# Kernel optimization log

Hardware: AMD Instinct MI355X
Metric: run time of the kernel (lower is better)

Reference implementation:

```python
import jax, jax.numpy as jnp
import numpy as np
from jax import lax

B, N_PER = 8, 4096          # clouds, points per cloud (batch vector is uniform)
RATIO, RADIUS, K = 0.25, 0.2, 64
N_SAMPLE = int(N_PER * RATIO)
C_IN, H = 64, 128               # input feature dim, MLP hidden/out dim


def setup_inputs() -> dict:
    key = jax.random.key(0)
    k = jax.random.split(key, 6)
    N = B * N_PER
    x = jax.random.normal(k[0], (N, C_IN), jnp.float32)
    pos = jax.random.uniform(k[1], (N, 3), jnp.float32)
    batch = jnp.repeat(jnp.arange(B, dtype=jnp.int32), N_PER)
    s1 = 1.0 / np.sqrt(C_IN + 3)
    s2 = 1.0 / np.sqrt(H)
    W1 = jax.random.uniform(k[2], (C_IN + 3, H), jnp.float32, -s1, s1)
    b1 = jax.random.uniform(k[3], (H,), jnp.float32, -s1, s1)
    W2 = jax.random.uniform(k[4], (H, H), jnp.float32, -s2, s2)
    b2 = jax.random.uniform(k[5], (H,), jnp.float32, -s2, s2)
    return {"x": x, "pos": pos, "W1": W1, "b1": b1, "W2": W2, "b2": b2, "batch": batch}


def _fps(pos_c):
    # Farthest point sampling on one cloud [n,3] -> [N_SAMPLE] int32 indices.
    # Sequential by nature: scan over sample steps, vectorized over all points.
    def step(carry, _):
        mind, last = carry
        d = jnp.sum((pos_c - pos_c[last]) ** 2, axis=-1)
        mind = jnp.minimum(mind, d)
        nxt = jnp.argmax(mind).astype(jnp.int32)
        return (mind, nxt), nxt

    init = (jnp.full((pos_c.shape[0],), 1e10, jnp.float32), jnp.int32(0))
    _, idxs = lax.scan(step, init, None, length=N_SAMPLE - 1)
    return jnp.concatenate([jnp.zeros((1,), jnp.int32), idxs])


def reference(x, pos, W1, b1, W2, b2, batch):
    # batch is uniform (N_PER points per cloud) so the flat [N,*] tensors
    # reshape to [B, N_PER, *]; this honors the per-batch fps/radius semantics.
    pos_b = pos.reshape(B, N_PER, 3)
    x_b = x.reshape(B, N_PER, C_IN)

    idx = jax.vmap(_fps)(pos_b)                                    # [B,S]
    pos_c = jnp.take_along_axis(pos_b, idx[..., None], axis=1)     # [B,S,3]

    # radius ball query: K nearest within RADIUS (cap max_num_neighbors=64)
    d2 = jnp.sum((pos_c[:, :, None, :] - pos_b[:, None, :, :]) ** 2, axis=-1)  # [B,S,n]
    neg_d, nbr = lax.top_k(-d2, K)                                 # [B,S,K]
    valid = (-neg_d) <= RADIUS ** 2                                # center itself always valid

    # gather neighbor features/positions via flat global indices
    gidx = (nbr + (jnp.arange(B, dtype=nbr.dtype) * N_PER)[:, None, None]).reshape(-1)
    x_j = x.reshape(B * N_PER, C_IN)[gidx].reshape(B, N_SAMPLE, K, C_IN)
    pos_j = pos.reshape(B * N_PER, 3)[gidx].reshape(B, N_SAMPLE, K, 3)

    # PointNetConv message: local_nn(concat(x_j, pos_j - pos_i)), max aggregation
    feat = jnp.concatenate([x_j, pos_j - pos_c[:, :, None, :]], axis=-1)  # [B,S,K,C_IN+3]
    h = jax.nn.relu(feat @ W1 + b1)
    h = jax.nn.relu(h @ W2 + b2)                                   # [B,S,K,H]
    h = jnp.where(valid[..., None], h, -1e9)
    x_out = jnp.max(h, axis=2).reshape(B * N_SAMPLE, H)

    pos_out = pos_c.reshape(B * N_SAMPLE, 3)
    batch_out = jnp.repeat(jnp.arange(B, dtype=jnp.int32), N_SAMPLE)
    return x_out, pos_out, batch_out
```

## Files before the change

kernel.cpp:

```cpp
#include <hip/hip_runtime.h>

#define NB 8
#define N_PER 4096
#define N_SAMPLE 1024
#define KNN 64
#define CIN 64
#define HD 128
#define R2F 0.04f
#define LIST_CAP 384
#define STR 136

typedef __attribute__((ext_vector_type(8))) short bf16x8;
typedef __attribute__((ext_vector_type(4))) float f32x4;

__device__ __forceinline__ unsigned short f2bf(float f) {
    const unsigned u = __float_as_uint(f);
    return (unsigned short)((u + 0x7fff + ((u >> 16) & 1)) >> 16);
}

template <int CTRL>
__device__ __forceinline__ unsigned long long dpp_shift_u64(unsigned long long k) {
    const unsigned lo = (unsigned)k;
    const unsigned hi = (unsigned)(k >> 32);
    const unsigned olo =
        (unsigned)__builtin_amdgcn_update_dpp(0, (int)lo, CTRL, 0xf, 0xf, false);
    const unsigned ohi =
        (unsigned)__builtin_amdgcn_update_dpp(0, (int)hi, CTRL, 0xf, 0xf, false);
    return ((unsigned long long)ohi << 32) | olo;
}
__device__ __forceinline__ unsigned long long wave_max_u64(unsigned long long k) {
    unsigned long long o;
    o = dpp_shift_u64<0x111>(k); k = o > k ? o : k;
    o = dpp_shift_u64<0x112>(k); k = o > k ? o : k;
    o = dpp_shift_u64<0x114>(k); k = o > k ? o : k;
    o = dpp_shift_u64<0x118>(k); k = o > k ? o : k;
    o = dpp_shift_u64<0x142>(k); k = o > k ? o : k;
    o = dpp_shift_u64<0x143>(k); k = o > k ? o : k;
    return k;
}

template <int CTRL, int RMASK>
__device__ __forceinline__ int dpp_add_step(int v) {
    const int o = __builtin_amdgcn_update_dpp(0, v, CTRL, RMASK, 0xf, false);
    return v + o;
}
__device__ __forceinline__ int wave_incl_scan(int v) {
    v = dpp_add_step<0x111, 0xf>(v);
    v = dpp_add_step<0x112, 0xf>(v);
    v = dpp_add_step<0x114, 0xf>(v);
    v = dpp_add_step<0x118, 0xf>(v);
    v = dpp_add_step<0x142, 0xa>(v);
    v = dpp_add_step<0x143, 0xc>(v);
    return v;
}

#define GBLOCKS ((NB * N_PER) / 2)
__global__ __launch_bounds__(256) void fps_g_kernel(const float* __restrict__ pos,
                                                    const float* __restrict__ x,
                                                    const float* __restrict__ W1,
                                                    const float* __restrict__ b1,
                                                    const float* __restrict__ W2,
                                                    float* __restrict__ g,
                                                    short* __restrict__ w2t,
                                                    int* __restrict__ idx_out,
                                                    float* __restrict__ pos_out,
                                                    float* __restrict__ batch_out) {
    __shared__ float pxyz[N_PER * 3];
    __shared__ __align__(16) unsigned long long pkey[2][4];
    __shared__ int lhist[N_SAMPLE];
    const int t = threadIdx.x;

    if (blockIdx.x >= NB + GBLOCKS) {
        const int base = (int)(blockIdx.x - (NB + GBLOCKS)) * 2048 + t * 8;
#pragma unroll
        for (int i = 0; i < 8; ++i) {
            const int idx = base + i;
            const int n = idx >> 7, k = idx & 127;
            w2t[idx] = (short)f2bf(W2[k * HD + n]);
        }
        return;
    }

    if (blockIdx.x >= NB) {
        const int n0 = (int)(blockIdx.x - NB) * 2;
        if (t < 2 * CIN) pxyz[t] = x[(size_t)n0 * CIN + t];
        if (t < 6) pxyz[512 + t] = pos[(size_t)n0 * 3 + t];
        __syncthreads();
        const int lp = t >> 7;
        const int h = t & 127;
        float acc = b1[h];
        const float* xv = pxyz + lp * CIN;
#pragma unroll 8
        for (int c = 0; c < CIN; ++c) acc += xv[c] * W1[c * HD + h];
        const float* pv = pxyz + 512 + lp * 3;
#pragma unroll
        for (int d = 0; d < 3; ++d) acc += pv[d] * W1[(CIN + d) * HD + h];
        g[(size_t)(n0 + lp) * HD + h] = acc;
        return;
    }

    const int b = blockIdx.x;
    const float* posb = pos + (size_t)b * N_PER * 3;
    for (int i = t; i < N_PER * 3; i += 256) pxyz[i] = posb[i];
    if (t == 0) lhist[0] = 0;
    __syncthreads();

    float rx[16], ry[16], rz[16], mind[16];
#pragma unroll
    for (int k = 0; k < 16; ++k) {
        const int p = t + (k << 8);
        rx[k] = pxyz[p * 3 + 0];
        ry[k] = pxyz[p * 3 + 1];
        rz[k] = pxyz[p * 3 + 2];
        mind[k] = 1e10f;
    }
    int last = 0;

    for (int s = 1; s < N_SAMPLE; ++s) {
        const float* lp3 = pxyz + last * 3;
        const float lx = lp3[0], ly = lp3[1], lz = lp3[2];
        float bv = -1.0f;
        int bi = 0x7fffffff;
#pragma unroll
        for (int k = 0; k < 16; ++k) {
            const float dx = rx[k] - lx;
            const float dy = ry[k] - ly;
            const float dz = rz[k] - lz;
            const float d = __fadd_rn(__fadd_rn(__fmul_rn(dx, dx), __fmul_rn(dy, dy)),
                                      __fmul_rn(dz, dz));
            const float m = fminf(mind[k], d);
            mind[k] = m;
            if (m > bv) { bv = m; bi = t + (k << 8); }
        }
        unsigned long long key =
            ((unsigned long long)__float_as_uint(bv) << 32) | (unsigned)(~bi);
        key = wave_max_u64(key);

        const int par = s & 1;
        if ((t & 63) == 63) pkey[par][t >> 6] = key;
        __syncthreads();
        const ulonglong2* pk2 = (const ulonglong2*)(&pkey[par][0]);
        const ulonglong2 A = pk2[0], Bq = pk2[1];
        unsigned long long f0 = A.x > A.y ? A.x : A.y;
        const unsigned long long f1 = Bq.x > Bq.y ? Bq.x : Bq.y;
        f0 = f0 > f1 ? f0 : f1;
        last = (int)(~(unsigned)f0);
        if (t == (s & 255)) lhist[s] = last;
    }
    __syncthreads();

    for (int i = t; i < N_SAMPLE; i += 256) {
        const int li = lhist[i];
        idx_out[b * N_SAMPLE + i] = b * N_PER + li;
        pos_out[(size_t)(b * N_SAMPLE + i) * 3 + 0] = pxyz[li * 3 + 0];
        pos_out[(size_t)(b * N_SAMPLE + i) * 3 + 1] = pxyz[li * 3 + 1];
        pos_out[(size_t)(b * N_SAMPLE + i) * 3 + 2] = pxyz[li * 3 + 2];
        batch_out[b * N_SAMPLE + i] = (float)b;
    }
}

__global__ __launch_bounds__(256) void main_kernel(const float* __restrict__ pos,
                                                   const float* __restrict__ W1,
                                                   const short* __restrict__ W2T,
                                                   const float* __restrict__ b2,
                                                   const float* __restrict__ g,
                                                   const int* __restrict__ idx_in,
                                                   float* __restrict__ x_out) {
    __shared__ short h1b[KNN * STR];
    __shared__ unsigned long long keys[LIST_CAP + 8];
    __shared__ int sel[KNN];
    __shared__ float pcW[HD];
    __shared__ float cp[3];
    __shared__ __align__(16) int wtot[4];
    __shared__ float stripmax[4][HD];

    const int t = threadIdx.x;
    const int s = blockIdx.x;
    const int b = s >> 10;
    const int gci = idx_in[s];
    if (t < 3) cp[t] = pos[(size_t)gci * 3 + t];
    if (t < KNN) sel[t] = 0;
    __syncthreads();

    if (t < HD) {
        pcW[t] = cp[0] * W1[CIN * HD + t] + cp[1] * W1[(CIN + 1) * HD + t] +
                 cp[2] * W1[(CIN + 2) * HD + t];
    }

    const float cx = cp[0], cy = cp[1], cz = cp[2];
    const size_t base = (size_t)b * N_PER;
    const int lane = t & 63;
    const int w = t >> 6;

    float d2r[16];
    int nh = 0;
#pragma unroll
    for (int k = 0; k < 16; ++k) {
        const int p = t + (k << 8);
        const float* pp = pos + (base + p) * 3;
        const float dx = pp[0] - cx;
        const float dy = pp[1] - cy;
        const float dz = pp[2] - cz;
        const float d2 = __fadd_rn(__fadd_rn(__fmul_rn(dx, dx), __fmul_rn(dy, dy)),
                                   __fmul_rn(dz, dz));
        d2r[k] = d2;
        nh += (d2 <= R2F) ? 1 : 0;
    }
    const int incl = wave_incl_scan(nh);
    if (lane == 63) wtot[w] = incl;
    __syncthreads();
    const int4 wt = *(const int4*)(&wtot[0]);
    const int tot = wt.x + wt.y + wt.z + wt.w;
    int slot = incl - nh;
    if (w > 0) slot += wt.x;
    if (w > 1) slot += wt.y;
    if (w > 2) slot += wt.z;
#pragma unroll
    for (int k = 0; k < 16; ++k) {
        if (d2r[k] <= R2F) {
            if (slot < LIST_CAP)
                keys[slot] = ((unsigned long long)__float_as_uint(d2r[k]) << 32) |
                             (unsigned)(t + (k << 8));
            ++slot;
        }
    }
    const int C = min(tot, LIST_CAP);
    const int Cp = (C + 7) & ~7;
    if (t < Cp - C) keys[C + t] = ~0ull;
    __syncthreads();
    const int M = min(C, KNN);

    for (int e = t; e < C; e += 256) {
        const unsigned long long ke = keys[e];
        int rank = 0;
        for (int q = 0; q < Cp; q += 8) {
#pragma unroll
            for (int j = 0; j < 8; ++j) rank += (keys[q + j] < ke) ? 1 : 0;
        }
        if (rank < KNN) sel[rank] = (int)(ke & 0xFFFFFFFFull);
    }
    __syncthreads();

    for (int lin = t; lin < KNN * (HD / 2); lin += 256) {
        const int m = lin >> 6;
        const int hp = lin & 63;
        float v0 = 0.0f, v1 = 0.0f;
        if (m < M) {
            const float2 gv = *(const float2*)(g + (base + sel[m]) * HD + 2 * hp);
            v0 = fmaxf(gv.x - pcW[2 * hp], 0.0f);
            v1 = fmaxf(gv.y - pcW[2 * hp + 1], 0.0f);
        }
        const unsigned pk = (unsigned)f2bf(v0) | ((unsigned)f2bf(v1) << 16);
        *(unsigned*)(&h1b[m * STR + 2 * hp]) = pk;
    }
    __syncthreads();

    const int row = lane & 15;
    const int kg = lane >> 4;

    bf16x8 afr[4];
#pragma unroll
    for (int kc = 0; kc < 4; ++kc)
        afr[kc] = *(const bf16x8*)(&h1b[(w * 16 + row) * STR + kc * 32 + kg * 8]);

#pragma unroll
    for (int nt = 0; nt < 8; ++nt) {
        f32x4 acc = {0.0f, 0.0f, 0.0f, 0.0f};
#pragma unroll
        for (int kc = 0; kc < 4; ++kc) {
            const bf16x8 bfr =
                *(const bf16x8*)(W2T + (nt * 16 + row) * HD + kc * 32 + kg * 8);
            acc = __builtin_amdgcn_mfma_f32_16x16x32_bf16(afr[kc], bfr, acc, 0, 0, 0);
        }
        const float bb = b2[nt * 16 + row];
        float mxv = -1e9f;
#pragma unroll
        for (int r = 0; r < 4; ++r) {
            const int m = w * 16 + kg * 4 + r;
            const float v = fmaxf(acc[r] + bb, 0.0f);
            if (m < M) mxv = fmaxf(mxv, v);
        }
        mxv = fmaxf(mxv, __shfl_xor(mxv, 16));
        mxv = fmaxf(mxv, __shfl_xor(mxv, 32));
        if (lane < 16) stripmax[w][nt * 16 + lane] = mxv;
    }
    __syncthreads();
    if (t < HD) {
        const float v = fmaxf(fmaxf(stripmax[0][t], stripmax[1][t]),
                              fmaxf(stripmax[2][t], stripmax[3][t]));
        x_out[(size_t)s * HD + t] = v;
    }
}

extern "C" void kernel_launch(void* const* d_in, const int* in_sizes, int n_in,
                              void* d_out, int out_size, void* d_ws, size_t ws_size,
                              hipStream_t stream) {
    const float* x   = (const float*)d_in[0];
    const float* pos = (const float*)d_in[1];
    const float* W1  = (const float*)d_in[2];
    const float* b1  = (const float*)d_in[3];
    const float* W2  = (const float*)d_in[4];
    const float* b2  = (const float*)d_in[5];

    float* out = (float*)d_out;
    float* x_out     = out;
    float* pos_out   = out + (size_t)NB * N_SAMPLE * HD;
    float* batch_out = pos_out + (size_t)NB * N_SAMPLE * 3;

    int*   idx_ws = (int*)d_ws;
    short* w2t    = (short*)((char*)d_ws + 32768);
    float* g      = (float*)((char*)d_ws + 65536);

    fps_g_kernel<<<NB + GBLOCKS + 8, 256, 0, stream>>>(pos, x, W1, b1, W2, g, w2t,
                                                       idx_ws, pos_out, batch_out);
    main_kernel<<<NB * N_SAMPLE, 256, 0, stream>>>(pos, W1, w2t, b2, g, idx_ws, x_out);
}
```

Measured before the change: 844.5 us.

## Fuse FPS and ball-query MLP into one persistent kernel with flag streaming

Merges the two kernels into one persistent launch. Eight blocks run farthest point sampling and publish each sampled center through per-sample global flags, while 500 worker blocks first compute the layer-1 projection g. They then meet at a global counter barrier and consume centers as they appear, interleaved across clouds. Downstream radius/MLP work can therefore overlap the sequential FPS instead of waiting for it to finish. In exchange it adds spin-wait polling, a memset, and a reliance on all blocks being co-resident for the grid barrier to avoid deadlock.

```diff
diff --git a/kernel.cpp b/kernel.cpp
--- a/kernel.cpp
+++ b/kernel.cpp
@@ -9,6 +9,12 @@
 #define R2F 0.04f
 #define LIST_CAP 384
 #define STR 136
+#define NFPS 8
+#define NWK 500
+#define GRID (NFPS + NWK)
+#define GCHUNK 66
+#define NPTS (NB * N_PER)
+#define NTASK (NB * N_SAMPLE)
 
 typedef __attribute__((ext_vector_type(8))) short bf16x8;
 typedef __attribute__((ext_vector_type(4))) float f32x4;
@@ -54,241 +60,268 @@
     return v;
 }
 
-#define GBLOCKS ((NB * N_PER) / 2)
-__global__ __launch_bounds__(256) void fps_g_kernel(const float* __restrict__ pos,
-                                                    const float* __restrict__ x,
-                                                    const float* __restrict__ W1,
-                                                    const float* __restrict__ b1,
-                                                    const float* __restrict__ W2,
-                                                    float* __restrict__ g,
-                                                    short* __restrict__ w2t,
-                                                    int* __restrict__ idx_out,
-                                                    float* __restrict__ pos_out,
-                                                    float* __restrict__ batch_out) {
-    __shared__ float pxyz[N_PER * 3];
-    __shared__ __align__(16) unsigned long long pkey[2][4];
-    __shared__ int lhist[N_SAMPLE];
+union SMem {
+    struct {
+        float pxyz[N_PER * 3];
+        unsigned long long pkey[2][4];
+    } f;
+    struct {
+        unsigned long long keys[LIST_CAP + 8];
+        short h1b[KNN * STR];
+        int sel[KNN];
+        float pcW[HD];
+        float stripmax[4][HD];
+        float gx[2 * CIN];
+        float gp[8];
+        int wtot[4];
+        int bcast;
+    } m;
+};
+
+__global__ __launch_bounds__(256, 2) void fused_kernel(
+    const float* __restrict__ pos, const float* __restrict__ x,
+    const float* __restrict__ W1, const float* __restrict__ b1,
+    const float* __restrict__ W2, const float* __restrict__ b2,
+    float* __restrict__ g, short* __restrict__ w2t, int* __restrict__ flags,
+    unsigned* __restrict__ gdone, float* __restrict__ x_out,
+    float* __restrict__ pos_out, float* __restrict__ batch_out) {
+    __shared__ SMem sm;
     const int t = threadIdx.x;
 
-    if (blockIdx.x >= NB + GBLOCKS) {
-        const int base = (int)(blockIdx.x - (NB + GBLOCKS)) * 2048 + t * 8;
-#pragma unroll
-        for (int i = 0; i < 8; ++i) {
-            const int idx = base + i;
-            const int n = idx >> 7, k = idx & 127;
-            w2t[idx] = (short)f2bf(W2[k * HD + n]);
+    if (blockIdx.x < NFPS) {
+        const int b = blockIdx.x;
+        const float* posb = pos + (size_t)b * N_PER * 3;
+        float* pxyz = sm.f.pxyz;
+        for (int i = t; i < N_PER * 3; i += 256) pxyz[i] = posb[i];
+        __syncthreads();
+
+        float rx[16], ry[16], rz[16], mind[16];
+#pragma unroll
+        for (int k = 0; k < 16; ++k) {
+            const int p = t + (k << 8);
+            rx[k] = pxyz[p * 3 + 0];
+            ry[k] = pxyz[p * 3 + 1];
+            rz[k] = pxyz[p * 3 + 2];
+            mind[k] = 1e10f;
+        }
+        int last = 0;
+        if (t == 0) {
+            __hip_atomic_store(&flags[b * N_SAMPLE], b * N_PER + 1, __ATOMIC_RELAXED,
+                               __HIP_MEMORY_SCOPE_AGENT);
+            pos_out[(size_t)(b * N_SAMPLE) * 3 + 0] = pxyz[0];
+            pos_out[(size_t)(b * N_SAMPLE) * 3 + 1] = pxyz[1];
+            pos_out[(size_t)(b * N_SAMPLE) * 3 + 2] = pxyz[2];
+            batch_out[b * N_SAMPLE] = (float)b;
+        }
+
+        for (int s = 1; s < N_SAMPLE; ++s) {
+            const float* lp3 = pxyz + last * 3;
+            const float lx = lp3[0], ly = lp3[1], lz = lp3[2];
+            float bv = -1.0f;
+            int bi = 0x7fffffff;
+#pragma unroll
+            for (int k = 0; k < 16; ++k) {
+                const float dx = rx[k] - lx;
+                const float dy = ry[k] - ly;
+                const float dz = rz[k] - lz;
+                const float d = __fadd_rn(
+                    __fadd_rn(__fmul_rn(dx, dx), __fmul_rn(dy, dy)), __fmul_rn(dz, dz));
+                const float m = fminf(mind[k], d);
+                mind[k] = m;
+                if (m > bv) { bv = m; bi = t + (k << 8); }
+            }
+            unsigned long long key =
+                ((unsigned long long)__float_as_uint(bv) << 32) | (unsigned)(~bi);
+            key = wave_max_u64(key);
+
+            const int par = s & 1;
+            if ((t & 63) == 63) sm.f.pkey[par][t >> 6] = key;
+            __syncthreads();
+            const ulonglong2* pk2 = (const ulonglong2*)(&sm.f.pkey[par][0]);
+            const ulonglong2 A = pk2[0], Bq = pk2[1];
+            unsigned long long f0 = A.x > A.y ? A.x : A.y;
+            const unsigned long long f1 = Bq.x > Bq.y ? Bq.x : Bq.y;
+            f0 = f0 > f1 ? f0 : f1;
+            last = (int)(~(unsigned)f0);
+            if (t == (s & 255)) {
+                __hip_atomic_store(&flags[b * N_SAMPLE + s], b * N_PER + last + 1,
+                                   __ATOMIC_RELAXED, __HIP_MEMORY_SCOPE_AGENT);
+                pos_out[(size_t)(b * N_SAMPLE + s) * 3 + 0] = pxyz[last * 3 + 0];
+                pos_out[(size_t)(b * N_SAMPLE + s) * 3 + 1] = pxyz[last * 3 + 1];
+                pos_out[(size_t)(b * N_SAMPLE + s) * 3 + 2] = pxyz[last * 3 + 2];
+                batch_out[b * N_SAMPLE + s] = (float)b;
+            }
         }
         return;
     }
 
-    if (blockIdx.x >= NB) {
-        const int n0 = (int)(blockIdx.x - NB) * 2;
-        if (t < 2 * CIN) pxyz[t] = x[(size_t)n0 * CIN + t];
-        if (t < 6) pxyz[512 + t] = pos[(size_t)n0 * 3 + t];
-        __syncthreads();
-        const int lp = t >> 7;
-        const int h = t & 127;
-        float acc = b1[h];
-        const float* xv = pxyz + lp * CIN;
+    const int w = (int)blockIdx.x - NFPS;
+
+    if (w < 64) {
+        const int idx = w * 256 + t;
+        w2t[idx] = (short)f2bf(W2[(idx & 127) * HD + (idx >> 7)]);
+    }
+    {
+        const int p0 = w * GCHUNK;
+        const int p1 = min(NPTS, p0 + GCHUNK);
+        for (int pp = p0; pp < p1; pp += 2) {
+            if (t < 2 * CIN && (size_t)pp * CIN + t < (size_t)NPTS * CIN)
+                sm.m.gx[t] = x[(size_t)pp * CIN + t];
+            if (t < 6 && pp * 3 + t < NPTS * 3) sm.m.gp[t] = pos[pp * 3 + t];
+            __syncthreads();
+            const int lp = t >> 7;
+            const int h = t & 127;
+            if (pp + lp < p1) {
+                float acc = b1[h];
+                const float* xv = sm.m.gx + lp * CIN;
 #pragma unroll 8
-        for (int c = 0; c < CIN; ++c) acc += xv[c] * W1[c * HD + h];
-        const float* pv = pxyz + 512 + lp * 3;
-#pragma unroll
-        for (int d = 0; d < 3; ++d) acc += pv[d] * W1[(CIN + d) * HD + h];
-        g[(size_t)(n0 + lp) * HD + h] = acc;
-        return;
-    }
-
-    const int b = blockIdx.x;
-    const float* posb = pos + (size_t)b * N_PER * 3;
-    for (int i = t; i < N_PER * 3; i += 256) pxyz[i] = posb[i];
-    if (t == 0) lhist[0] = 0;
+                for (int c = 0; c < CIN; ++c) acc += xv[c] * W1[c * HD + h];
+                const float* pv = sm.m.gp + lp * 3;
+#pragma unroll
+                for (int d = 0; d < 3; ++d) acc += pv[d] * W1[(CIN + d) * HD + h];
+                g[(size_t)(pp + lp) * HD + h] = acc;
+            }
+            __syncthreads();
+        }
+    }
+    __threadfence();
     __syncthreads();
-
-    float rx[16], ry[16], rz[16], mind[16];
-#pragma unroll
-    for (int k = 0; k < 16; ++k) {
-        const int p = t + (k << 8);
-        rx[k] = pxyz[p * 3 + 0];
-        ry[k] = pxyz[p * 3 + 1];
-        rz[k] = pxyz[p * 3 + 2];
-        mind[k] = 1e10f;
-    }
-    int last = 0;
-
-    for (int s = 1; s < N_SAMPLE; ++s) {
-        const float* lp3 = pxyz + last * 3;
-        const float lx = lp3[0], ly = lp3[1], lz = lp3[2];
-        float bv = -1.0f;
-        int bi = 0x7fffffff;
+    if (t == 0)
+        __hip_atomic_fetch_add(gdone, 1u, __ATOMIC_RELEASE, __HIP_MEMORY_SCOPE_AGENT);
+    if (t == 0) {
+        while (__hip_atomic_load(gdone, __ATOMIC_ACQUIRE, __HIP_MEMORY_SCOPE_AGENT) <
+               (unsigned)NWK)
+            __builtin_amdgcn_s_sleep(32);
+    }
+    __syncthreads();
+
+    const int lane = t & 63;
+    const int wv = t >> 6;
+    for (int j = w; j < NTASK; j += NWK) {
+        const int i = j >> 3;
+        const int b = j & 7;
+        const int sidx = b * N_SAMPLE + i;
+        if (t == 0) {
+            int v;
+            while ((unsigned)((v = __hip_atomic_load(&flags[sidx], __ATOMIC_RELAXED,
+                                                     __HIP_MEMORY_SCOPE_AGENT)) -
+                              1) >= (unsigned)NPTS)
+                __builtin_amdgcn_s_sleep(8);
+            sm.m.bcast = v - 1;
+        }
+        if (t < KNN) sm.m.sel[t] = 0;
+        __syncthreads();
+        const int gci = sm.m.bcast;
+        const float cx = pos[(size_t)gci * 3 + 0];
+        const float cy = pos[(size_t)gci * 3 + 1];
+        const float cz = pos[(size_t)gci * 3 + 2];
+        if (t < HD) {
+            sm.m.pcW[t] = cx * W1[CIN * HD + t] + cy * W1[(CIN + 1) * HD + t] +
+                          cz * W1[(CIN + 2) * HD + t];
+        }
+        const size_t base = (size_t)b * N_PER;
+
+        float d2r[16];
+        int nh = 0;
 #pragma unroll
         for (int k = 0; k < 16; ++k) {
-            const float dx = rx[k] - lx;
-            const float dy = ry[k] - ly;
-            const float dz = rz[k] - lz;
-            const float d = __fadd_rn(__fadd_rn(__fmul_rn(dx, dx), __fmul_rn(dy, dy)),
-                                      __fmul_rn(dz, dz));
-            const float m = fminf(mind[k], d);
-            mind[k] = m;
-            if (m > bv) { bv = m; bi = t + (k << 8); }
-        }
-        unsigned long long key =
-            ((unsigned long long)__float_as_uint(bv) << 32) | (unsigned)(~bi);
-        key = wave_max_u64(key);
-
-        const int par = s & 1;
-        if ((t & 63) == 63) pkey[par][t >> 6] = key;
-        __syncthreads();
-        const ulonglong2* pk2 = (const ulonglong2*)(&pkey[par][0]);
-        const ulonglong2 A = pk2[0], Bq = pk2[1];
-        unsigned long long f0 = A.x > A.y ? A.x : A.y;
-        const unsigned long long f1 = Bq.x > Bq.y ? Bq.x : Bq.y;
-        f0 = f0 > f1 ? f0 : f1;
-        last = (int)(~(unsigned)f0);
-        if (t == (s & 255)) lhist[s] = last;
-    }
-    __syncthreads();
-
-    for (int i = t; i < N_SAMPLE; i += 256) {
-        const int li = lhist[i];
-        idx_out[b * N_SAMPLE + i] = b * N_PER + li;
-        pos_out[(size_t)(b * N_SAMPLE + i) * 3 + 0] = pxyz[li * 3 + 0];
-        pos_out[(size_t)(b * N_SAMPLE + i) * 3 + 1] = pxyz[li * 3 + 1];
-        pos_out[(size_t)(b * N_SAMPLE + i) * 3 + 2] = pxyz[li * 3 + 2];
-        batch_out[b * N_SAMPLE + i] = (float)b;
-    }
-}
-
-__global__ __launch_bounds__(256) void main_kernel(const float* __restrict__ pos,
-                                                   const float* __restrict__ W1,
-                                                   const short* __restrict__ W2T,
-                                                   const float* __restrict__ b2,
-                                                   const float* __restrict__ g,
-                                                   const int* __restrict__ idx_in,
-                                                   float* __restrict__ x_out) {
-    __shared__ short h1b[KNN * STR];
-    __shared__ unsigned long long keys[LIST_CAP + 8];
-    __shared__ int sel[KNN];
-    __shared__ float pcW[HD];
-    __shared__ float cp[3];
-    __shared__ __align__(16) int wtot[4];
-    __shared__ float stripmax[4][HD];
-
-    const int t = threadIdx.x;
-    const int s = blockIdx.x;
-    const int b = s >> 10;
-    const int gci = idx_in[s];
-    if (t < 3) cp[t] = pos[(size_t)gci * 3 + t];
-    if (t < KNN) sel[t] = 0;
-    __syncthreads();
-
-    if (t < HD) {
-        pcW[t] = cp[0] * W1[CIN * HD + t] + cp[1] * W1[(CIN + 1) * HD + t] +
-                 cp[2] * W1[(CIN + 2) * HD + t];
-    }
-
-    const float cx = cp[0], cy = cp[1], cz = cp[2];
-    const size_t base = (size_t)b * N_PER;
-    const int lane = t & 63;
-    const int w = t >> 6;
-
-    float d2r[16];
-    int nh = 0;
-#pragma unroll
-    for (int k = 0; k < 16; ++k) {
-        const int p = t + (k << 8);
-        const float* pp = pos + (base + p) * 3;
-        const float dx = pp[0] - cx;
-        const float dy = pp[1] - cy;
-        const float dz = pp[2] - cz;
-        const float d2 = __fadd_rn(__fadd_rn(__fmul_rn(dx, dx), __fmul_rn(dy, dy)),
-                                   __fmul_rn(dz, dz));
-        d2r[k] = d2;
-        nh += (d2 <= R2F) ? 1 : 0;
-    }
-    const int incl = wave_incl_scan(nh);
-    if (lane == 63) wtot[w] = incl;
-    __syncthreads();
-    const int4 wt = *(const int4*)(&wtot[0]);
-    const int tot = wt.x + wt.y + wt.z + wt.w;
-    int slot = incl - nh;
-    if (w > 0) slot += wt.x;
-    if (w > 1) slot += wt.y;
-    if (w > 2) slot += wt.z;
-#pragma unroll
-    for (int k = 0; k < 16; ++k) {
-        if (d2r[k] <= R2F) {
-            if (slot < LIST_CAP)
-                keys[slot] = ((unsigned long long)__float_as_uint(d2r[k]) << 32) |
-                             (unsigned)(t + (k << 8));
-            ++slot;
-        }
-    }
-    const int C = min(tot, LIST_CAP);
-    const int Cp = (C + 7) & ~7;
-    if (t < Cp - C) keys[C + t] = ~0ull;
-    __syncthreads();
-    const int M = min(C, KNN);
-
-    for (int e = t; e < C; e += 256) {
-        const unsigned long long ke = keys[e];
-        int rank = 0;
-        for (int q = 0; q < Cp; q += 8) {
-#pragma unroll
-            for (int j = 0; j < 8; ++j) rank += (keys[q + j] < ke) ? 1 : 0;
-        }
-        if (rank < KNN) sel[rank] = (int)(ke & 0xFFFFFFFFull);
-    }
-    __syncthreads();
-
-    for (int lin = t; lin < KNN * (HD / 2); lin += 256) {
-        const int m = lin >> 6;
-        const int hp = lin & 63;
-        float v0 = 0.0f, v1 = 0.0f;
-        if (m < M) {
-            const float2 gv = *(const float2*)(g + (base + sel[m]) * HD + 2 * hp);
-            v0 = fmaxf(gv.x - pcW[2 * hp], 0.0f);
-            v1 = fmaxf(gv.y - pcW[2 * hp + 1], 0.0f);
-        }
-        const unsigned pk = (unsigned)f2bf(v0) | ((unsigned)f2bf(v1) << 16);
-        *(unsigned*)(&h1b[m * STR + 2 * hp]) = pk;
-    }
-    __syncthreads();
-
-    const int row = lane & 15;
-    const int kg = lane >> 4;
-
-    bf16x8 afr[4];
-#pragma unroll
-    for (int kc = 0; kc < 4; ++kc)
-        afr[kc] = *(const bf16x8*)(&h1b[(w * 16 + row) * STR + kc * 32 + kg * 8]);
-
-#pragma unroll
-    for (int nt = 0; nt < 8; ++nt) {
-        f32x4 acc = {0.0f, 0.0f, 0.0f, 0.0f};
-#pragma unroll
-        for (int kc = 0; kc < 4; ++kc) {
-            const bf16x8 bfr =
-                *(const bf16x8*)(W2T + (nt * 16 + row) * HD + kc * 32 + kg * 8);
-            acc = __builtin_amdgcn_mfma_f32_16x16x32_bf16(afr[kc], bfr, acc, 0, 0, 0);
-        }
-        const float bb = b2[nt * 16 + row];
-        float mxv = -1e9f;
-#pragma unroll
-        for (int r = 0; r < 4; ++r) {
-            const int m = w * 16 + kg * 4 + r;
-            const float v = fmaxf(acc[r] + bb, 0.0f);
-            if (m < M) mxv = fmaxf(mxv, v);
-        }
-        mxv = fmaxf(mxv, __shfl_xor(mxv, 16));
-        mxv = fmaxf(mxv, __shfl_xor(mxv, 32));
-        if (lane < 16) stripmax[w][nt * 16 + lane] = mxv;
-    }
-    __syncthreads();
-    if (t < HD) {
-        const float v = fmaxf(fmaxf(stripmax[0][t], stripmax[1][t]),
-                              fmaxf(stripmax[2][t], stripmax[3][t]));
-        x_out[(size_t)s * HD + t] = v;
+            const int p = t + (k << 8);
+            const float* pp = pos + (base + p) * 3;
+            const float dx = pp[0] - cx;
+            const float dy = pp[1] - cy;
+            const float dz = pp[2] - cz;
+            const float d2 = __fadd_rn(
+                __fadd_rn(__fmul_rn(dx, dx), __fmul_rn(dy, dy)), __fmul_rn(dz, dz));
+            d2r[k] = d2;
+            nh += (d2 <= R2F) ? 1 : 0;
+        }
+        const int incl = wave_incl_scan(nh);
+        if (lane == 63) sm.m.wtot[wv] = incl;
+        __syncthreads();
+        const int4 wt = *(const int4*)(&sm.m.wtot[0]);
+        const int tot = wt.x + wt.y + wt.z + wt.w;
+        int slot = incl - nh;
+        if (wv > 0) slot += wt.x;
+        if (wv > 1) slot += wt.y;
+        if (wv > 2) slot += wt.z;
+#pragma unroll
+        for (int k = 0; k < 16; ++k) {
+            if (d2r[k] <= R2F) {
+                if (slot < LIST_CAP)
+                    sm.m.keys[slot] =
+                        ((unsigned long long)__float_as_uint(d2r[k]) << 32) |
+                        (unsigned)(t + (k << 8));
+                ++slot;
+            }
+        }
+        const int C = min(tot, LIST_CAP);
+        const int Cp = (C + 7) & ~7;
+        if (t < Cp - C) sm.m.keys[C + t] = ~0ull;
+        __syncthreads();
+        const int M = min(C, KNN);
+
+        for (int e = t; e < C; e += 256) {
+            const unsigned long long ke = sm.m.keys[e];
+            int rank = 0;
+            for (int q = 0; q < Cp; q += 8) {
+#pragma unroll
+                for (int jj = 0; jj < 8; ++jj) rank += (sm.m.keys[q + jj] < ke) ? 1 : 0;
+            }
+            if (rank < KNN) sm.m.sel[rank] = (int)(ke & 0xFFFFFFFFull);
+        }
+        __syncthreads();
+
+        for (int lin = t; lin < KNN * (HD / 2); lin += 256) {
+            const int m = lin >> 6;
+            const int hp = lin & 63;
+            float v0 = 0.0f, v1 = 0.0f;
+            if (m < M) {
+                const float2 gv =
+                    *(const float2*)(g + (base + sm.m.sel[m]) * HD + 2 * hp);
+                v0 = fmaxf(gv.x - sm.m.pcW[2 * hp], 0.0f);
+                v1 = fmaxf(gv.y - sm.m.pcW[2 * hp + 1], 0.0f);
+            }
+            const unsigned pk = (unsigned)f2bf(v0) | ((unsigned)f2bf(v1) << 16);
+            *(unsigned*)(&sm.m.h1b[m * STR + 2 * hp]) = pk;
+        }
+        __syncthreads();
+
+        const int row = lane & 15;
+        const int kg = lane >> 4;
+        bf16x8 afr[4];
+#pragma unroll
+        for (int kc = 0; kc < 4; ++kc)
+            afr[kc] =
+                *(const bf16x8*)(&sm.m.h1b[(wv * 16 + row) * STR + kc * 32 + kg * 8]);
+
+#pragma unroll
+        for (int nt = 0; nt < 8; ++nt) {
+            f32x4 acc = {0.0f, 0.0f, 0.0f, 0.0f};
+#pragma unroll
+            for (int kc = 0; kc < 4; ++kc) {
+                const bf16x8 bfr =
+                    *(const bf16x8*)(w2t + (nt * 16 + row) * HD + kc * 32 + kg * 8);
+                acc = __builtin_amdgcn_mfma_f32_16x16x32_bf16(afr[kc], bfr, acc, 0, 0, 0);
+            }
+            const float bb = b2[nt * 16 + row];
+            float mxv = -1e9f;
+#pragma unroll
+            for (int r = 0; r < 4; ++r) {
+                const int m = wv * 16 + kg * 4 + r;
+                const float v = fmaxf(acc[r] + bb, 0.0f);
+                if (m < M) mxv = fmaxf(mxv, v);
+            }
+            mxv = fmaxf(mxv, __shfl_xor(mxv, 16));
+            mxv = fmaxf(mxv, __shfl_xor(mxv, 32));
+            if (lane < 16) sm.m.stripmax[wv][nt * 16 + lane] = mxv;
+        }
+        __syncthreads();
+        if (t < HD) {
+            const float v = fmaxf(fmaxf(sm.m.stripmax[0][t], sm.m.stripmax[1][t]),
+                                  fmaxf(sm.m.stripmax[2][t], sm.m.stripmax[3][t]));
+            x_out[(size_t)sidx * HD + t] = v;
+        }
+        __syncthreads();
     }
 }
 
@@ -307,11 +340,13 @@
     float* pos_out   = out + (size_t)NB * N_SAMPLE * HD;
     float* batch_out = pos_out + (size_t)NB * N_SAMPLE * 3;
 
-    int*   idx_ws = (int*)d_ws;
-    short* w2t    = (short*)((char*)d_ws + 32768);
-    float* g      = (float*)((char*)d_ws + 65536);
-
-    fps_g_kernel<<<NB + GBLOCKS + 8, 256, 0, stream>>>(pos, x, W1, b1, W2, g, w2t,
-                                                       idx_ws, pos_out, batch_out);
-    main_kernel<<<NB * N_SAMPLE, 256, 0, stream>>>(pos, W1, w2t, b2, g, idx_ws, x_out);
-}
+    short*    w2t   = (short*)d_ws;
+    int*      flags = (int*)((char*)d_ws + 32768);
+    unsigned* gdone = (unsigned*)((char*)d_ws + 65536);
+    float*    g     = (float*)((char*)d_ws + 69632);
+
+    hipMemsetAsync((char*)d_ws + 32768, 0, 36864, stream);
+
+    fused_kernel<<<GRID, 256, 0, stream>>>(pos, x, W1, b1, W2, b2, g, w2t, flags,
+                                           gdone, x_out, pos_out, batch_out);
+}
```

New measurement: 744.7 us. 1.13x faster.
